# Kernel tuning notes

Hardware: AMD Instinct MI355X
Metric: run time of the kernel (lower is better)

Reference implementation:

```python
import jax, jax.numpy as jnp
import numpy as np

N = 50000      # nodes per graph
E = 800000     # edges per graph (avg degree 16)
IN = 128       # in_channels == hidden_channels
HID = 128      # out_channels (heads=1)
R = 8          # num_relations
NEG = 0.2      # PyG RGATConv default negative_slope


def setup_inputs() -> dict:
    key = jax.random.key(0)
    ks = jax.random.split(key, 14)
    s_w = (2.0 / (IN + HID)) ** 0.5  # glorot-ish scale
    return {
        "x_one": jax.random.normal(ks[0], (N, IN), jnp.float32),
        "edge_index_one": jax.random.randint(ks[1], (2, E), 0, N),
        "edge_type_one": jax.random.randint(ks[2], (E,), 0, R),
        "x_two": jax.random.normal(ks[3], (N, IN), jnp.float32),
        "edge_index_two": jax.random.randint(ks[4], (2, E), 0, N),
        "edge_type_two": jax.random.randint(ks[5], (E,), 0, R),
        "W1": jax.random.normal(ks[6], (R, IN, HID), jnp.float32) * s_w,
        "q1": jax.random.normal(ks[7], (HID, 1), jnp.float32) * s_w,
        "k1": jax.random.normal(ks[8], (HID, 1), jnp.float32) * s_w,
        "b1": jnp.zeros((HID,), jnp.float32),
        "W2": jax.random.normal(ks[9], (R, IN, HID), jnp.float32) * s_w,
        "q2": jax.random.normal(ks[10], (HID, 1), jnp.float32) * s_w,
        "k2": jax.random.normal(ks[11], (HID, 1), jnp.float32) * s_w,
        "b2": jnp.zeros((HID,), jnp.float32),
    }


def _rgat(x, edge_index, edge_type, W, q, k, b):
    """PyG RGATConv (heads=1, additive-self-attention, across-relation)."""
    n = x.shape[0]
    src, dst = edge_index[0], edge_index[1]
    # per-relation linear transform of all nodes: [R, N, HID]
    xt = jnp.einsum('nd,rdo->rno', x, W)
    out_i = xt[edge_type, dst]   # [E, HID] transformed target (x_i W_r)
    out_j = xt[edge_type, src]   # [E, HID] transformed source (x_j W_r)
    qi = out_i @ q               # [E, 1]
    kj = out_j @ k               # [E, 1]
    alpha = jax.nn.leaky_relu(qi + kj, NEG)
    # scatter-softmax over incoming edges of each dst node
    amax = jax.ops.segment_max(alpha, dst, num_segments=n)
    amax = jnp.where(jnp.isfinite(amax), amax, 0.0)
    ex = jnp.exp(alpha - amax[dst])
    denom = jax.ops.segment_sum(ex, dst, num_segments=n) + 1e-16
    a = ex / denom[dst]          # [E, 1]
    # weighted scatter-add aggregation + bias
    out = jax.ops.segment_sum(a * out_j, dst, num_segments=n) + b
    return out


def reference(x_one, edge_index_one, edge_type_one,
              x_two, edge_index_two, edge_type_two,
              W1, q1, k1, b1, W2, q2, k2, b2):
    o1 = jax.nn.relu(_rgat(x_one, edge_index_one, edge_type_one, W1, q1, k1, b1))
    o2 = jax.nn.relu(_rgat(x_two, edge_index_two, edge_type_two, W2, q2, k2, b2))
    return (o1, o2)
```

## Files before the change

kernel.cpp:

```cpp
#include <hip/hip_runtime.h>


typedef unsigned short u16;
typedef __attribute__((ext_vector_type(8))) short short8;
typedef __attribute__((ext_vector_type(4))) float floatx4;
typedef __attribute__((ext_vector_type(4))) float float4v;
typedef __attribute__((ext_vector_type(4))) unsigned uint4v;

#define BCAP 8192

__device__ __forceinline__ u16 f2bf(float f) {
  union { float f; unsigned u; } v; v.f = f;
  unsigned r = v.u + 0x7FFFu + ((v.u >> 16) & 1u);
  return (u16)(r >> 16);
}
__device__ __forceinline__ float bflo(unsigned v) {
  union { unsigned u; float f; } c; c.u = v << 16; return c.f;
}
__device__ __forceinline__ float bfhi(unsigned v) {
  union { unsigned u; float f; } c; c.u = v & 0xffff0000u; return c.f;
}
__device__ __forceinline__ unsigned cvtpk(float lo, float hi) {
  unsigned r;
  asm("v_cvt_pk_bf16_f32 %0, %1, %2" : "=v"(r) : "v"(lo), "v"(hi));
  return r;
}

__global__ void k_prep_wb(const float* __restrict__ W1, const float* __restrict__ W2,
                          u16* __restrict__ Wb, int KK) {
  int t = blockIdx.x * 256 + threadIdx.x;
  int lane = t & 63, nt = (t >> 6) & 7, kk = t >> 9;
  if (kk >= KK) return;
  const float* W = blockIdx.y ? W2 : W1;
  u16* out = Wb + (size_t)blockIdx.y * KK * 4096;
  int q = lane >> 4, m16 = lane & 15;
  int c = nt * 16 + m16;
  short8 v;
#pragma unroll
  for (int j = 0; j < 8; ++j) {
    int k = kk * 32 + q * 8 + j;
    v[j] = (short)f2bf(W[(size_t)k * 128 + c]);
  }
  *(short8*)(out + (size_t)t * 8) = v;
}

__global__ void __launch_bounds__(256) k_prep_bqk(
    const float* __restrict__ W1, const float* __restrict__ q1,
    const float* __restrict__ k1, const float* __restrict__ W2,
    const float* __restrict__ q2, const float* __restrict__ k2,
    u16* __restrict__ Bqk) {
  int idx = blockIdx.x * 256 + threadIdx.x;
  int j = idx & 7, lane = (idx >> 3) & 63, kk = (idx >> 9) & 3, g = idx >> 11;
  int k = kk * 32 + ((lane >> 4) & 3) * 8 + j;
  int n = lane & 15;
  const float* W = g ? W2 : W1;
  const float* vec = (n < 8) ? (g ? q2 : q1) : (g ? k2 : k1);
  const float* row = W + ((size_t)(n & 7) * 128 + k) * 128;
  float s = 0.f;
#pragma unroll
  for (int o = 0; o < 128; o += 4) {
    float4v wv = *(const float4v*)(row + o);
    float4v qv = *(const float4v*)(vec + o);
    s += wv.x * qv.x + wv.y * qv.y + wv.z * qv.z + wv.w * qv.w;
  }
  Bqk[idx] = f2bf(s);
}

__global__ void __launch_bounds__(256) k_bin2(
    const int* __restrict__ ei1, const int* __restrict__ et1,
    const int* __restrict__ ei2, const int* __restrict__ et2,
    int* __restrict__ bcnt, uint2* __restrict__ staged, int N, int E, int NB) {
  __shared__ int hist[512];
  __shared__ int basev[512];
  __shared__ int runstart[512];
  __shared__ unsigned sta[4096 * 2];
  int tid = threadIdx.x;
  int E2 = 2 * E;
  int e0 = blockIdx.x * 4096;
  int cnt2 = min(4096, E2 - e0);
  for (int i = tid; i < 512; i += 256) hist[i] = 0;
  __syncthreads();
  int dstg[16], srcet[16], rank[16];
#pragma unroll
  for (int j = 0; j < 16; ++j) {
    int e = e0 + j * 256 + tid;
    dstg[j] = -1;
    if (e < E2) {
      int g = e >= E;
      int el = e - (g ? E : 0);
      const int* ei = g ? ei2 : ei1;
      int s = ei[el], d = ei[E + el];
      int etv = (g ? et2 : et1)[el];
      dstg[j] = g * N + d;
      srcet[j] = (s << 3) | etv;
      rank[j] = atomicAdd(&hist[dstg[j] >> 8], 1);
    }
  }
  __syncthreads();
  basev[tid] = hist[tid];
  basev[tid + 256] = hist[tid + 256];
  __syncthreads();
  for (int off = 1; off < 512; off <<= 1) {
    int i0 = tid, i1 = tid + 256;
    int v0 = (i0 >= off) ? basev[i0 - off] : 0;
    int v1 = (i1 >= off) ? basev[i1 - off] : 0;
    __syncthreads();
    basev[i0] += v0; basev[i1] += v1;
    __syncthreads();
  }
  for (int i = tid; i < NB; i += 256)
    if (hist[i] > 0) runstart[i] = atomicAdd(&bcnt[i], hist[i]);
  __syncthreads();
#pragma unroll
  for (int j = 0; j < 16; ++j)
    if (dstg[j] >= 0) {
      int b = dstg[j] >> 8;
      int slot = basev[b] - hist[b] + rank[j];
      sta[slot * 2] = (unsigned)dstg[j];
      sta[slot * 2 + 1] = (unsigned)srcet[j];
    }
  __syncthreads();
  for (int i = tid; i < cnt2; i += 256) {
    unsigned dg = sta[i * 2], se = sta[i * 2 + 1];
    int b = (int)(dg >> 8);
    int dest = (b << 13) + runstart[b] + (i - (basev[b] - hist[b]));
    staged[dest] = make_uint2(dg, se);
  }
}

__global__ void __launch_bounds__(256) k_scatter3(
    const uint2* __restrict__ staged, const int* __restrict__ bcnt,
    int* __restrict__ offs, int* __restrict__ ends, int* __restrict__ csr,
    int N2) {
  __shared__ int hist[256];
  __shared__ int sd[256];
  __shared__ int cur[256];
  int b = blockIdx.x, tid = threadIdx.x;
  int nb0 = b << 8;
  int nnode = min(256, N2 - nb0);
  int s0 = b << 13;
  int cnt = bcnt[b];
  hist[tid] = 0;
  __syncthreads();
  for (int i = tid; i < cnt; i += 256)
    atomicAdd(&hist[(int)staged[s0 + i].x - nb0], 1);
  __syncthreads();
  int v = hist[tid];
  sd[tid] = v; __syncthreads();
  for (int off = 1; off < 256; off <<= 1) {
    int t = (tid >= off) ? sd[tid - off] : 0;
    __syncthreads();
    sd[tid] += t;
    __syncthreads();
  }
  int ex = sd[tid] - v;
  if (tid < nnode) {
    offs[nb0 + tid] = s0 + ex;
    ends[nb0 + tid] = s0 + ex + v;
  }
  cur[tid] = ex;
  __syncthreads();
  for (int i = tid; i < cnt; i += 256) {
    uint2 en = staged[s0 + i];
    int node = (int)en.x - nb0;
    int sl = atomicAdd(&cur[node], 1);
    csr[s0 + sl] = (int)en.y;
  }
}

__global__ void __launch_bounds__(256) k_gemm_xt(
    const float* __restrict__ x, const u16* __restrict__ Wb,
    const u16* __restrict__ Bqk, u16* __restrict__ xt,
    float* __restrict__ sq, float* __restrict__ sk,
    int N, int R, int node_base) {
  __shared__ u16 st[4][2][2048];
  int wave = threadIdx.x >> 6, lane = threadIdx.x & 63;
  int m0 = blockIdx.x * 64 + wave * 16;
  int rbase = blockIdx.y * 4;
  int q = lane >> 4, m16 = lane & 15;
  int node = m0 + m16;
  int srow = (node < N) ? node : N - 1;
  short8 bfrag[4];
#pragma unroll
  for (int kk = 0; kk < 4; ++kk) {
    const float* ap = x + (size_t)srow * 128 + kk * 32 + q * 8;
    float4v f0 = *(const float4v*)ap;
    float4v f1 = *(const float4v*)(ap + 4);
    union { unsigned u[4]; short8 s; } pb;
    pb.u[0] = cvtpk(f0.x, f0.y); pb.u[1] = cvtpk(f0.z, f0.w);
    pb.u[2] = cvtpk(f1.x, f1.y); pb.u[3] = cvtpk(f1.z, f1.w);
    bfrag[kk] = pb.s;
  }
  if (blockIdx.y == 0) {
    floatx4 accq = (floatx4){0.f, 0.f, 0.f, 0.f};
#pragma unroll
    for (int kk = 0; kk < 4; ++kk) {
      short8 aq = *(const short8*)(Bqk + (size_t)kk * 512 + lane * 8);
      accq = __builtin_amdgcn_mfma_f32_16x16x32_bf16(aq, bfrag[kk], accq, 0, 0, 0);
    }
    if (node < N) {
      float* dst = (q < 2 ? sq : sk) + (size_t)(node_base + node) * 8 + (q & 1) * 4;
      *(float4v*)dst = (float4v){accq[0], accq[1], accq[2], accq[3]};
    }
  }
#pragma unroll
  for (int rr = 0; rr < 4; ++rr) {
    int r = rbase + rr;
    u16* s = st[wave][rr & 1];
    floatx4 acc[8];
#pragma unroll
    for (int nt = 0; nt < 8; ++nt) acc[nt] = (floatx4){0.f, 0.f, 0.f, 0.f};
#pragma unroll
    for (int kk = 0; kk < 4; ++kk) {
      const u16* wbp = Wb + ((size_t)((r * 4 + kk) * 8) * 64 + lane) * 8;
#pragma unroll
      for (int nt = 0; nt < 8; ++nt) {
        short8 a = *(const short8*)(wbp + nt * 512);
        acc[nt] = __builtin_amdgcn_mfma_f32_16x16x32_bf16(a, bfrag[kk], acc[nt], 0, 0, 0);
      }
    }
#pragma unroll
    for (int nt = 0; nt < 8; ++nt) {
      union { unsigned u[2]; unsigned long long ull; } pk;
      pk.u[0] = cvtpk(acc[nt][0], acc[nt][1]);
      pk.u[1] = cvtpk(acc[nt][2], acc[nt][3]);
      int c16 = 2 * nt + (q >> 1);
      *(unsigned long long*)(s + (((m16 << 4) + (c16 ^ m16)) << 3) + ((q & 1) << 2)) = pk.ull;
    }
#pragma unroll
    for (int it = 0; it < 4; ++it) {
      int rl = it * 4 + q;
      int gm = m0 + rl;
      if (gm < N) {
        uint4v vv = *(const uint4v*)(s + (((rl << 4) + (m16 ^ rl)) << 3));
        *(uint4v*)(xt + ((size_t)r * N + gm) * 128 + m16 * 8) = vv;
      }
    }
  }
}

__global__ void __launch_bounds__(256) k_aggregate(
    const int* __restrict__ csr, const int* __restrict__ offs,
    const int* __restrict__ ends,
    const float* __restrict__ sq, const float* __restrict__ sk,
    const u16* __restrict__ xt, const float* __restrict__ bias,
    float* __restrict__ out, int N, int node_base) {
  int nl = blockIdx.x * 4 + (threadIdx.x >> 6);
  int lane = threadIdx.x & 63;
  if (nl >= N) return;
  int node = node_base + nl;
  int start = offs[node], end = ends[node];
  const float* sqn = sq + (size_t)node * 8;

  float al[8]; int pl[8];
  float m = -INFINITY;
  {
    int c = 0;
    for (int i = start + lane; i < end; i += 64, ++c) {
      int p = csr[i]; int s = p >> 3, e = p & 7;
      float a = sqn[e] + sk[(size_t)(node_base + s) * 8 + e];
      a = (a > 0.f) ? a : 0.2f * a;
      if (c < 8) { al[c] = a; pl[c] = p; }
      m = fmaxf(m, a);
    }
  }
#pragma unroll
  for (int off = 32; off; off >>= 1) m = fmaxf(m, __shfl_xor(m, off));

  float ssum = 0.f;
  {
    int c = 0;
    for (int i = start + lane; i < end; i += 64, ++c) {
      float a;
      if (c < 8) a = al[c];
      else {
        int p = csr[i]; int s = p >> 3, e = p & 7;
        a = sqn[e] + sk[(size_t)(node_base + s) * 8 + e];
        a = (a > 0.f) ? a : 0.2f * a;
      }
      ssum += __expf(a - m);
    }
  }
#pragma unroll
  for (int off = 32; off; off >>= 1) ssum += __shfl_xor(ssum, off);
  float inv = 1.f / (ssum + 1e-16f);

  float acc0 = 0.f, acc1 = 0.f;
  const char* xtb = (const char*)xt;
  int c = 0;
  for (int base = start; base < end; base += 64, ++c) {
    int cnt = min(64, end - base);
    float w = 0.f; int b = 0;
    {
      int i = base + lane;
      if (i < end) {
        int p; float a;
        if (c < 8) { p = pl[c]; a = al[c]; }
        else {
          p = csr[i]; int s = p >> 3, e = p & 7;
          a = sqn[e] + sk[(size_t)(node_base + s) * 8 + e];
          a = (a > 0.f) ? a : 0.2f * a;
        }
        w = __expf(a - m) * inv;
        b = ((p & 7) * N + (p >> 3)) << 8;
      }
    }
    int j = 0;
    for (; j + 3 < cnt; j += 4) {
      float w0 = __shfl(w, j), w1 = __shfl(w, j + 1),
            w2 = __shfl(w, j + 2), w3 = __shfl(w, j + 3);
      int b0 = __shfl(b, j), b1 = __shfl(b, j + 1),
          b2 = __shfl(b, j + 2), b3 = __shfl(b, j + 3);
      unsigned v0 = *(const unsigned*)(xtb + b0 + lane * 4);
      unsigned v1 = *(const unsigned*)(xtb + b1 + lane * 4);
      unsigned v2 = *(const unsigned*)(xtb + b2 + lane * 4);
      unsigned v3 = *(const unsigned*)(xtb + b3 + lane * 4);
      acc0 += w0 * bflo(v0); acc1 += w0 * bfhi(v0);
      acc0 += w1 * bflo(v1); acc1 += w1 * bfhi(v1);
      acc0 += w2 * bflo(v2); acc1 += w2 * bfhi(v2);
      acc0 += w3 * bflo(v3); acc1 += w3 * bfhi(v3);
    }
    for (; j < cnt; ++j) {
      float w0 = __shfl(w, j);
      int b0 = __shfl(b, j);
      unsigned v0 = *(const unsigned*)(xtb + b0 + lane * 4);
      acc0 += w0 * bflo(v0); acc1 += w0 * bfhi(v0);
    }
  }
  float o0 = fmaxf(acc0 + bias[lane * 2], 0.f);
  float o1 = fmaxf(acc1 + bias[lane * 2 + 1], 0.f);
  union { float f[2]; unsigned long long u; } pk;
  pk.f[0] = o0; pk.f[1] = o1;
  __builtin_nontemporal_store(pk.u,
      (unsigned long long*)(out + (size_t)nl * 128 + lane * 2));
}

extern "C" void kernel_launch(void* const* d_in, const int* in_sizes, int n_in,
                              void* d_out, int out_size, void* d_ws, size_t ws_size,
                              hipStream_t stream) {
  const float* x1 = (const float*)d_in[0];
  const int* ei1 = (const int*)d_in[1];
  const int* et1 = (const int*)d_in[2];
  const float* x2 = (const float*)d_in[3];
  const int* ei2 = (const int*)d_in[4];
  const int* et2 = (const int*)d_in[5];
  const float* W1 = (const float*)d_in[6];
  const float* q1 = (const float*)d_in[7];
  const float* k1 = (const float*)d_in[8];
  const float* b1 = (const float*)d_in[9];
  const float* W2 = (const float*)d_in[10];
  const float* q2 = (const float*)d_in[11];
  const float* k2 = (const float*)d_in[12];
  const float* b2 = (const float*)d_in[13];

  const int N = in_sizes[0] / 128;
  const int E = in_sizes[1] / 2;
  const int R = in_sizes[6] / (128 * 128);
  const int KK = R * 4;
  const int N2 = 2 * N;
  const int NB = (N2 + 255) >> 8;

  size_t off = 0;
  char* w = (char*)d_ws;
  auto carve = [&](size_t bytes) -> void* {
    void* p = w + off;
    off += (bytes + 255) & ~(size_t)255;
    return p;
  };
  u16* Wb = (u16*)carve((size_t)2 * KK * 4096 * 2);
  u16* Bqk = (u16*)carve((size_t)2 * 4 * 64 * 8 * 2);
  float* sq = (float*)carve((size_t)N2 * 8 * 4);
  float* sk = (float*)carve((size_t)N2 * 8 * 4);
  int* offs = (int*)carve((size_t)N2 * 4);
  int* ends = (int*)carve((size_t)N2 * 4);
  int* bcnt = (int*)carve(512 * 4);
  int* csr = (int*)carve((size_t)NB * BCAP * 4);
  u16* xt = (u16*)carve((size_t)R * N * 128 * 2);
  uint2* staged = (uint2*)xt;
  if (off > ws_size) return;
  if ((size_t)NB * BCAP * 8 > (size_t)R * N * 128 * 2) return;

  const int nbin = (2 * E + 4095) / 4096;

  hipMemsetAsync(bcnt, 0, 512 * 4, stream);
  k_prep_wb<<<dim3((KK * 512 + 255) / 256, 2), dim3(256), 0, stream>>>(W1, W2, Wb, KK);
  k_prep_bqk<<<dim3(16), dim3(256), 0, stream>>>(W1, q1, k1, W2, q2, k2, Bqk);
  k_bin2<<<dim3(nbin), dim3(256), 0, stream>>>(ei1, et1, ei2, et2, bcnt, staged, N, E, NB);
  k_scatter3<<<dim3(NB), dim3(256), 0, stream>>>(staged, bcnt, offs, ends, csr, N2);

  for (int g = 0; g < 2; ++g) {
    const float* x = g ? x2 : x1;
    const float* bv = g ? b2 : b1;
    float* outp = (float*)d_out + (size_t)g * N * 128;
    k_gemm_xt<<<dim3((N + 63) / 64, 2), dim3(256), 0, stream>>>(
        x, Wb + (size_t)g * KK * 4096, Bqk + (size_t)g * 2048, xt,
        sq, sk, N, R, g * N);
    k_aggregate<<<dim3((N + 3) / 4), dim3(256), 0, stream>>>(
        csr, offs, ends, sq, sk, xt, bv, outp, N, g * N);
  }
}
```

Baseline: 340.9 us.

## Fuse prep kernels and co-schedule edge binning with first graph's GEMM

Merges the W-to-bf16 packing, q/k projection and bcnt zeroing into one prep kernel, replacing a memset and two launches. Edge binning and graph one's per-relation transform GEMM now run as different block ranges of one launch, so the memory-bound sort overlaps the MFMA work. The staged edge buffer gets its own workspace allocation instead of aliasing xt, because both are now written at the same time. This uses more workspace, and the combined kernel's shared memory is a union sized for the larger of the two roles.

```diff
diff --git a/kernel.cpp b/kernel.cpp
--- a/kernel.cpp
+++ b/kernel.cpp
@@ -26,105 +26,200 @@
   return r;
 }
 
-__global__ void k_prep_wb(const float* __restrict__ W1, const float* __restrict__ W2,
-                          u16* __restrict__ Wb, int KK) {
-  int t = blockIdx.x * 256 + threadIdx.x;
-  int lane = t & 63, nt = (t >> 6) & 7, kk = t >> 9;
-  if (kk >= KK) return;
-  const float* W = blockIdx.y ? W2 : W1;
-  u16* out = Wb + (size_t)blockIdx.y * KK * 4096;
-  int q = lane >> 4, m16 = lane & 15;
-  int c = nt * 16 + m16;
-  short8 v;
-#pragma unroll
-  for (int j = 0; j < 8; ++j) {
-    int k = kk * 32 + q * 8 + j;
-    v[j] = (short)f2bf(W[(size_t)k * 128 + c]);
-  }
-  *(short8*)(out + (size_t)t * 8) = v;
-}
-
-__global__ void __launch_bounds__(256) k_prep_bqk(
+__global__ void __launch_bounds__(256) k_prep(
     const float* __restrict__ W1, const float* __restrict__ q1,
     const float* __restrict__ k1, const float* __restrict__ W2,
     const float* __restrict__ q2, const float* __restrict__ k2,
-    u16* __restrict__ Bqk) {
-  int idx = blockIdx.x * 256 + threadIdx.x;
-  int j = idx & 7, lane = (idx >> 3) & 63, kk = (idx >> 9) & 3, g = idx >> 11;
-  int k = kk * 32 + ((lane >> 4) & 3) * 8 + j;
-  int n = lane & 15;
-  const float* W = g ? W2 : W1;
-  const float* vec = (n < 8) ? (g ? q2 : q1) : (g ? k2 : k1);
-  const float* row = W + ((size_t)(n & 7) * 128 + k) * 128;
-  float s = 0.f;
-#pragma unroll
-  for (int o = 0; o < 128; o += 4) {
-    float4v wv = *(const float4v*)(row + o);
-    float4v qv = *(const float4v*)(vec + o);
-    s += wv.x * qv.x + wv.y * qv.y + wv.z * qv.z + wv.w * qv.w;
-  }
-  Bqk[idx] = f2bf(s);
-}
-
-__global__ void __launch_bounds__(256) k_bin2(
+    u16* __restrict__ Wb, u16* __restrict__ Bqk, int* __restrict__ bcnt,
+    int KK, int wbHalf) {
+  int b = blockIdx.x, tid = threadIdx.x;
+  int wbBlocks = 2 * wbHalf;
+  if (b < wbBlocks) {
+    int gy = b >= wbHalf;
+    int t = (b - gy * wbHalf) * 256 + tid;
+    int lane = t & 63, nt = (t >> 6) & 7, kk = t >> 9;
+    if (kk >= KK) return;
+    const float* W = gy ? W2 : W1;
+    u16* out = Wb + (size_t)gy * KK * 4096;
+    int q = lane >> 4, m16 = lane & 15;
+    int c = nt * 16 + m16;
+    short8 v;
+#pragma unroll
+    for (int j = 0; j < 8; ++j) {
+      int k = kk * 32 + q * 8 + j;
+      v[j] = (short)f2bf(W[(size_t)k * 128 + c]);
+    }
+    *(short8*)(out + (size_t)t * 8) = v;
+  } else {
+    int bb = b - wbBlocks;
+    if (bb < 2) {
+      int z = bb * 256 + tid;
+      bcnt[z] = 0;
+    }
+    int idx = bb * 256 + tid;
+    int j = idx & 7, lane = (idx >> 3) & 63, kk = (idx >> 9) & 3, g = idx >> 11;
+    int k = kk * 32 + ((lane >> 4) & 3) * 8 + j;
+    int n = lane & 15;
+    const float* W = g ? W2 : W1;
+    const float* vec = (n < 8) ? (g ? q2 : q1) : (g ? k2 : k1);
+    const float* row = W + ((size_t)(n & 7) * 128 + k) * 128;
+    float s = 0.f;
+#pragma unroll
+    for (int o = 0; o < 128; o += 4) {
+      float4v wv = *(const float4v*)(row + o);
+      float4v qv = *(const float4v*)(vec + o);
+      s += wv.x * qv.x + wv.y * qv.y + wv.z * qv.z + wv.w * qv.w;
+    }
+    Bqk[idx] = f2bf(s);
+  }
+}
+
+struct BinSmem {
+  int hist[512];
+  int basev[512];
+  int runstart[512];
+  unsigned sta[8192];
+};
+union SortGemmSmem {
+  BinSmem bn;
+  u16 st[4][2][2048];
+};
+
+__global__ void __launch_bounds__(256) k_sortgemm(
     const int* __restrict__ ei1, const int* __restrict__ et1,
     const int* __restrict__ ei2, const int* __restrict__ et2,
-    int* __restrict__ bcnt, uint2* __restrict__ staged, int N, int E, int NB) {
-  __shared__ int hist[512];
-  __shared__ int basev[512];
-  __shared__ int runstart[512];
-  __shared__ unsigned sta[4096 * 2];
+    int* __restrict__ bcnt, uint2* __restrict__ staged,
+    const float* __restrict__ x, const u16* __restrict__ Wb,
+    const u16* __restrict__ Bqk, u16* __restrict__ xt,
+    float* __restrict__ sq, float* __restrict__ sk,
+    int N, int E, int NB, int R, int nbin, int gx) {
+  __shared__ SortGemmSmem sm;
   int tid = threadIdx.x;
-  int E2 = 2 * E;
-  int e0 = blockIdx.x * 4096;
-  int cnt2 = min(4096, E2 - e0);
-  for (int i = tid; i < 512; i += 256) hist[i] = 0;
-  __syncthreads();
-  int dstg[16], srcet[16], rank[16];
-#pragma unroll
-  for (int j = 0; j < 16; ++j) {
-    int e = e0 + j * 256 + tid;
-    dstg[j] = -1;
-    if (e < E2) {
-      int g = e >= E;
-      int el = e - (g ? E : 0);
-      const int* ei = g ? ei2 : ei1;
-      int s = ei[el], d = ei[E + el];
-      int etv = (g ? et2 : et1)[el];
-      dstg[j] = g * N + d;
-      srcet[j] = (s << 3) | etv;
-      rank[j] = atomicAdd(&hist[dstg[j] >> 8], 1);
-    }
-  }
-  __syncthreads();
-  basev[tid] = hist[tid];
-  basev[tid + 256] = hist[tid + 256];
-  __syncthreads();
-  for (int off = 1; off < 512; off <<= 1) {
-    int i0 = tid, i1 = tid + 256;
-    int v0 = (i0 >= off) ? basev[i0 - off] : 0;
-    int v1 = (i1 >= off) ? basev[i1 - off] : 0;
-    __syncthreads();
-    basev[i0] += v0; basev[i1] += v1;
-    __syncthreads();
-  }
-  for (int i = tid; i < NB; i += 256)
-    if (hist[i] > 0) runstart[i] = atomicAdd(&bcnt[i], hist[i]);
-  __syncthreads();
-#pragma unroll
-  for (int j = 0; j < 16; ++j)
-    if (dstg[j] >= 0) {
-      int b = dstg[j] >> 8;
-      int slot = basev[b] - hist[b] + rank[j];
-      sta[slot * 2] = (unsigned)dstg[j];
-      sta[slot * 2 + 1] = (unsigned)srcet[j];
-    }
-  __syncthreads();
-  for (int i = tid; i < cnt2; i += 256) {
-    unsigned dg = sta[i * 2], se = sta[i * 2 + 1];
-    int b = (int)(dg >> 8);
-    int dest = (b << 13) + runstart[b] + (i - (basev[b] - hist[b]));
-    staged[dest] = make_uint2(dg, se);
+
+  if ((int)blockIdx.x < nbin) {
+    int* hist = sm.bn.hist;
+    int* basev = sm.bn.basev;
+    int* runstart = sm.bn.runstart;
+    unsigned* sta = sm.bn.sta;
+    int E2 = 2 * E;
+    int e0 = blockIdx.x * 4096;
+    int cnt2 = min(4096, E2 - e0);
+    for (int i = tid; i < 512; i += 256) hist[i] = 0;
+    __syncthreads();
+    int dstg[16], srcet[16], rank[16];
+#pragma unroll
+    for (int j = 0; j < 16; ++j) {
+      int e = e0 + j * 256 + tid;
+      dstg[j] = -1;
+      if (e < E2) {
+        int g = e >= E;
+        int el = e - (g ? E : 0);
+        const int* ei = g ? ei2 : ei1;
+        int s = ei[el], d = ei[E + el];
+        int etv = (g ? et2 : et1)[el];
+        dstg[j] = g * N + d;
+        srcet[j] = (s << 3) | etv;
+        rank[j] = atomicAdd(&hist[dstg[j] >> 8], 1);
+      }
+    }
+    __syncthreads();
+    basev[tid] = hist[tid];
+    basev[tid + 256] = hist[tid + 256];
+    __syncthreads();
+    for (int off = 1; off < 512; off <<= 1) {
+      int i0 = tid, i1 = tid + 256;
+      int v0 = (i0 >= off) ? basev[i0 - off] : 0;
+      int v1 = (i1 >= off) ? basev[i1 - off] : 0;
+      __syncthreads();
+      basev[i0] += v0; basev[i1] += v1;
+      __syncthreads();
+    }
+    for (int i = tid; i < NB; i += 256)
+      if (hist[i] > 0) runstart[i] = atomicAdd(&bcnt[i], hist[i]);
+    __syncthreads();
+#pragma unroll
+    for (int j = 0; j < 16; ++j)
+      if (dstg[j] >= 0) {
+        int b = dstg[j] >> 8;
+        int slot = basev[b] - hist[b] + rank[j];
+        sta[slot * 2] = (unsigned)dstg[j];
+        sta[slot * 2 + 1] = (unsigned)srcet[j];
+      }
+    __syncthreads();
+    for (int i = tid; i < cnt2; i += 256) {
+      unsigned dg = sta[i * 2], se = sta[i * 2 + 1];
+      int b = (int)(dg >> 8);
+      int dest = (b << 13) + runstart[b] + (i - (basev[b] - hist[b]));
+      staged[dest] = make_uint2(dg, se);
+    }
+    return;
+  }
+
+  int f = blockIdx.x - nbin;
+  int bx = f % gx;
+  int by = f / gx;
+  int wave = tid >> 6, lane = tid & 63;
+  int m0 = bx * 64 + wave * 16;
+  int rbase = by * 4;
+  int q = lane >> 4, m16 = lane & 15;
+  int node = m0 + m16;
+  int srow = (node < N) ? node : N - 1;
+  short8 bfrag[4];
+#pragma unroll
+  for (int kk = 0; kk < 4; ++kk) {
+    const float* ap = x + (size_t)srow * 128 + kk * 32 + q * 8;
+    float4v f0 = *(const float4v*)ap;
+    float4v f1 = *(const float4v*)(ap + 4);
+    union { unsigned u[4]; short8 s; } pb;
+    pb.u[0] = cvtpk(f0.x, f0.y); pb.u[1] = cvtpk(f0.z, f0.w);
+    pb.u[2] = cvtpk(f1.x, f1.y); pb.u[3] = cvtpk(f1.z, f1.w);
+    bfrag[kk] = pb.s;
+  }
+  if (by == 0) {
+    floatx4 accq = (floatx4){0.f, 0.f, 0.f, 0.f};
+#pragma unroll
+    for (int kk = 0; kk < 4; ++kk) {
+      short8 aq = *(const short8*)(Bqk + (size_t)kk * 512 + lane * 8);
+      accq = __builtin_amdgcn_mfma_f32_16x16x32_bf16(aq, bfrag[kk], accq, 0, 0, 0);
+    }
+    if (node < N) {
+      float* dst = (q < 2 ? sq : sk) + (size_t)node * 8 + (q & 1) * 4;
+      *(float4v*)dst = (float4v){accq[0], accq[1], accq[2], accq[3]};
+    }
+  }
+#pragma unroll
+  for (int rr = 0; rr < 4; ++rr) {
+    int r = rbase + rr;
+    u16* s = sm.st[wave][rr & 1];
+    floatx4 acc[8];
+#pragma unroll
+    for (int nt = 0; nt < 8; ++nt) acc[nt] = (floatx4){0.f, 0.f, 0.f, 0.f};
+#pragma unroll
+    for (int kk = 0; kk < 4; ++kk) {
+      const u16* wbp = Wb + ((size_t)((r * 4 + kk) * 8) * 64 + lane) * 8;
+#pragma unroll
+      for (int nt = 0; nt < 8; ++nt) {
+        short8 a = *(const short8*)(wbp + nt * 512);
+        acc[nt] = __builtin_amdgcn_mfma_f32_16x16x32_bf16(a, bfrag[kk], acc[nt], 0, 0, 0);
+      }
+    }
+#pragma unroll
+    for (int nt = 0; nt < 8; ++nt) {
+      union { unsigned u[2]; unsigned long long ull; } pk;
+      pk.u[0] = cvtpk(acc[nt][0], acc[nt][1]);
+      pk.u[1] = cvtpk(acc[nt][2], acc[nt][3]);
+      int c16 = 2 * nt + (q >> 1);
+      *(unsigned long long*)(s + (((m16 << 4) + (c16 ^ m16)) << 3) + ((q & 1) << 2)) = pk.ull;
+    }
+#pragma unroll
+    for (int it = 0; it < 4; ++it) {
+      int rl = it * 4 + q;
+      int gm = m0 + rl;
+      if (gm < N) {
+        uint4v vv = *(const uint4v*)(s + (((rl << 4) + (m16 ^ rl)) << 3));
+        *(uint4v*)(xt + ((size_t)r * N + gm) * 128 + m16 * 8) = vv;
+      }
+    }
   }
 }
 
@@ -375,27 +470,25 @@
   int* ends = (int*)carve((size_t)N2 * 4);
   int* bcnt = (int*)carve(512 * 4);
   int* csr = (int*)carve((size_t)NB * BCAP * 4);
+  uint2* staged = (uint2*)carve((size_t)NB * BCAP * 8);
   u16* xt = (u16*)carve((size_t)R * N * 128 * 2);
-  uint2* staged = (uint2*)xt;
   if (off > ws_size) return;
-  if ((size_t)NB * BCAP * 8 > (size_t)R * N * 128 * 2) return;
 
   const int nbin = (2 * E + 4095) / 4096;
-
-  hipMemsetAsync(bcnt, 0, 512 * 4, stream);
-  k_prep_wb<<<dim3((KK * 512 + 255) / 256, 2), dim3(256), 0, stream>>>(W1, W2, Wb, KK);
-  k_prep_bqk<<<dim3(16), dim3(256), 0, stream>>>(W1, q1, k1, W2, q2, k2, Bqk);
-  k_bin2<<<dim3(nbin), dim3(256), 0, stream>>>(ei1, et1, ei2, et2, bcnt, staged, N, E, NB);
+  const int gx = (N + 63) / 64;
+  const int wbHalf = (KK * 512 + 255) / 256;
+
+  k_prep<<<dim3(2 * wbHalf + 16), dim3(256), 0, stream>>>(
+      W1, q1, k1, W2, q2, k2, Wb, Bqk, bcnt, KK, wbHalf);
+  k_sortgemm<<<dim3(nbin + 2 * gx), dim3(256), 0, stream>>>(
+      ei1, et1, ei2, et2, bcnt, staged,
+      x1, Wb, Bqk, xt, sq, sk, N, E, NB, R, nbin, gx);
   k_scatter3<<<dim3(NB), dim3(256), 0, stream>>>(staged, bcnt, offs, ends, csr, N2);
-
-  for (int g = 0; g < 2; ++g) {
-    const float* x = g ? x2 : x1;
-    const float* bv = g ? b2 : b1;
-    float* outp = (float*)d_out + (size_t)g * N * 128;
-    k_gemm_xt<<<dim3((N + 63) / 64, 2), dim3(256), 0, stream>>>(
-        x, Wb + (size_t)g * KK * 4096, Bqk + (size_t)g * 2048, xt,
-        sq, sk, N, R, g * N);
-    k_aggregate<<<dim3((N + 3) / 4), dim3(256), 0, stream>>>(
-        csr, offs, ends, sq, sk, xt, bv, outp, N, g * N);
-  }
-}
+  k_aggregate<<<dim3((N + 3) / 4), dim3(256), 0, stream>>>(
+      csr, offs, ends, sq, sk, xt, b1, (float*)d_out, N, 0);
+  k_gemm_xt<<<dim3(gx, 2), dim3(256), 0, stream>>>(
+      x2, Wb + (size_t)KK * 4096, Bqk + 2048, xt, sq, sk, N, R, N);
+  k_aggregate<<<dim3((N + 3) / 4), dim3(256), 0, stream>>>(
+      csr, offs, ends, sq, sk, xt, b2,
+      (float*)d_out + (size_t)N * 128, N, N);
+}
```

New measurement: 324.2 us. -4.9%, faster.
